# Kernel tuning notes

Measured on AMD Instinct MI355X. Metric: run time of the kernel, lower is better.

## Reference

```python
import jax, jax.numpy as jnp
import numpy as np

N_NODES = 100000
N_EDGES = 3200000
H, D = 3, 12  # heads, per-head dim; H*D == node_hidden_dim == 36
NEG_SLOPE = 0.2


def setup_inputs() -> dict:
    key = jax.random.key(0)
    ks = jax.random.split(key, 11)
    s = 0.1
    return {
        "node_features": jax.random.normal(ks[0], (N_NODES, 36), jnp.float32),
        "src": jax.random.randint(ks[1], (N_EDGES,), 0, N_NODES),
        "dst": jax.random.randint(ks[2], (N_EDGES,), 0, N_NODES),
        "lin0_w": jax.random.normal(ks[3], (36, 36), jnp.float32) * s,
        "lin0_b": jax.random.normal(ks[4], (36,), jnp.float32) * s,
        "fc_w": jax.random.normal(ks[5], (3, 36, 36), jnp.float32) * s,
        "attn_l": jax.random.normal(ks[6], (3, H, D), jnp.float32) * s,
        "attn_r": jax.random.normal(ks[7], (3, H, D), jnp.float32) * s,
        "gat_bias": jax.random.normal(ks[8], (3, 36), jnp.float32) * s,
        "out_w": jax.random.normal(ks[9], (36, 36), jnp.float32) * s,
        "out_b": jax.random.normal(ks[10], (36,), jnp.float32) * s,
    }


def _gat_layer(h, src, dst, fc_w, a_l, a_r, bias):
    n = h.shape[0]
    feat = (h @ fc_w).reshape(n, H, D)                      # (N,H,D)
    el = jnp.sum(feat * a_l, axis=-1)                       # (N,H)
    er = jnp.sum(feat * a_r, axis=-1)                       # (N,H)
    e = el[src] + er[dst]                                   # (E,H)
    e = jnp.where(e >= 0, e, NEG_SLOPE * e)                 # leaky_relu(0.2)
    # edge softmax over incoming edges of each dst node (numerically stable)
    m = jax.ops.segment_max(e, dst, num_segments=n)         # (N,H)
    m = jnp.where(jnp.isfinite(m), m, 0.0)                  # zero-degree guard
    ee = jnp.exp(e - m[dst])                                # (E,H)
    denom = jax.ops.segment_sum(ee, dst, num_segments=n)    # (N,H)
    alpha = ee / jnp.maximum(denom[dst], 1e-9)              # (E,H)
    msg = feat[src] * alpha[:, :, None]                     # (E,H,D)
    rst = jax.ops.segment_sum(msg, dst, num_segments=n)     # (N,H,D)
    # residual (Identity since in_feats == H*D) + bias, then ELU
    rst = rst + h.reshape(n, H, D) + bias.reshape(1, H, D)
    return jax.nn.elu(rst).reshape(n, H * D)


def reference(node_features, src, dst, lin0_w, lin0_b, fc_w, attn_l, attn_r, gat_bias, out_w, out_b):
    h = node_features @ lin0_w + lin0_b
    for l in range(3):
        h = _gat_layer(h, src, dst, fc_w[l], attn_l[l], attn_r[l], gat_bias[l])
    return h @ out_w + out_b
```

## Files before the change

### kernel.cpp

```cpp
#include <hip/hip_runtime.h>
#include <math.h>

#define HID 36
#define NH 3
#define HD 12
#define BSHIFT 13
#define NBUCK 13
#define PSHIFT 8
#define PCHUNK 8192
#define CSRCAP 4096

typedef _Float16 f16;
typedef unsigned short u16;


__global__ void hist2_kernel(const int* __restrict__ dst, int* __restrict__ M,
                             int E, int C, int np) {
    __shared__ int h[512];
    int t = threadIdx.x;
    int c = blockIdx.x;
    for (int i = t; i < 512; i += blockDim.x) h[i] = 0;
    __syncthreads();
    int i0 = c * PCHUNK;
    int i1 = min(i0 + PCHUNK, E);
    for (int i = i0 + t; i < i1; i += blockDim.x)
        atomicAdd(&h[dst[i] >> PSHIFT], 1);
    __syncthreads();
    for (int b = t; b < np; b += blockDim.x)
        M[(size_t)b * C + c] = h[b];
}

__global__ void base_scan_kernel(const int* __restrict__ M, int* __restrict__ BaseT,
                                 int* __restrict__ T, int C, int np) {
    __shared__ int tmp[512];
    int b = blockIdx.x;
    int t = threadIdx.x;
    int v = (t < C) ? M[(size_t)b * C + t] : 0;
    tmp[t] = v;
    __syncthreads();
    for (int ofs = 1; ofs < 512; ofs <<= 1) {
        int x = 0;
        if (t >= ofs) x = tmp[t - ofs];
        __syncthreads();
        tmp[t] += x;
        __syncthreads();
    }
    if (t < C) BaseT[(size_t)t * 512 + b] = tmp[t] - v;
    if (t == 511) T[b] = tmp[511];
}

__global__ void scan_small_kernel(const int* __restrict__ T, int* __restrict__ poff, int np) {
    __shared__ int tmp[512];
    int t = threadIdx.x;
    int v = (t < np) ? T[t] : 0;
    tmp[t] = v;
    __syncthreads();
    for (int ofs = 1; ofs < 512; ofs <<= 1) {
        int x = 0;
        if (t >= ofs) x = tmp[t - ofs];
        __syncthreads();
        tmp[t] += x;
        __syncthreads();
    }
    int excl = tmp[t] - v;
    if (t < np) poff[t] = excl;
    if (t == np - 1) poff[np] = excl + v;
}

__global__ void part_scatter_kernel(const int* __restrict__ src, const int* __restrict__ dst,
                                    const int* __restrict__ BaseT, const int* __restrict__ poff,
                                    int* __restrict__ part, int E, int np) {
    __shared__ int h[512];
    __shared__ int base[512];
    int t = threadIdx.x;
    int c = blockIdx.x;
    for (int i = t; i < 512; i += blockDim.x) h[i] = 0;
    for (int b = t; b < np; b += blockDim.x)
        base[b] = poff[b] + BaseT[(size_t)c * 512 + b];
    __syncthreads();
    int i0 = c * PCHUNK;
    int i1 = min(i0 + PCHUNK, E);
    for (int i = i0 + t; i < i1; i += blockDim.x) {
        int d = dst[i];
        int bin = d >> PSHIFT;
        int r = atomicAdd(&h[bin], 1);
        part[base[bin] + r] = (src[i] << PSHIFT) | (d & ((1 << PSHIFT) - 1));
    }
}

__global__ void bucket_csr_kernel(const int* __restrict__ part, const int* __restrict__ T,
                                  const int* __restrict__ poff,
                                  int* __restrict__ csr, int* __restrict__ off,
                                  u16* __restrict__ counts, int n, int E) {
    __shared__ int cnt[256 * NBUCK];
    __shared__ int psum[256];
    int p = blockIdx.x;
    int t = threadIdx.x;
    int dbase = p << PSHIFT;
    int nd = min(256, n - dbase);
    int nc = nd * NBUCK;
    for (int i = t; i < nc; i += blockDim.x) cnt[i] = 0;
    __syncthreads();
    int cnt_p = T[p];
    int e0 = poff[p];
    const int* pp = part + e0;
    for (int i = t; i < cnt_p; i += blockDim.x) {
        int e = pp[i];
        atomicAdd(&cnt[(e & 255) * NBUCK + ((e >> PSHIFT) >> BSHIFT)], 1);
    }
    __syncthreads();
    int sum = 0;
    if (t < nd) {
        for (int k = 0; k < NBUCK; ++k) {
            int c = cnt[t * NBUCK + k];
            cnt[t * NBUCK + k] = sum;
            sum += c;
        }
    }
    psum[t] = (t < nd) ? sum : 0;
    __syncthreads();
    for (int ofs = 1; ofs < 256; ofs <<= 1) {
        int x = 0;
        if (t >= ofs) x = psum[t - ofs];
        __syncthreads();
        psum[t] += x;
        __syncthreads();
    }
    int dexcl = (t > 0) ? psum[t - 1] : 0;
    int start = e0 + dexcl;
    if (t < nd) {
        for (int k = 0; k < NBUCK; ++k) cnt[t * NBUCK + k] += start;
        off[dbase + t] = start;
    }
    __syncthreads();
    for (int i = t; i < cnt_p; i += blockDim.x) {
        int e = pp[i];
        int s = e >> PSHIFT;
        int idx = (e & 255) * NBUCK + (s >> BSHIFT);
        int pos = atomicAdd(&cnt[idx], 1);
        csr[pos] = s * 48;
    }
    __syncthreads();
    if (t < nd) {
        union { u16 cc[16]; uint4 q[2]; } u;
        int prev = start;
        for (int k = 0; k < NBUCK; ++k) {
            int end = cnt[t * NBUCK + k];
            u.cc[k] = (u16)(end - prev);
            prev = end;
        }
        u.cc[13] = 0; u.cc[14] = 0; u.cc[15] = 0;
        uint4* cp = (uint4*)(counts + (size_t)(dbase + t) * 16);
        cp[0] = u.q[0];
        cp[1] = u.q[1];
    }
    if (p == 0 && t == 0) off[n] = E;
}


__device__ __forceinline__ void edge_accum(uint4 qa, uint4 qb, float ern,
                                           float& denom, float* acc) {
    union { uint4 q[2]; f16 hx[16]; } v;
    v.q[0] = qa;
    v.q[1] = qb;
    float e = (float)v.hx[12] + ern;
    e = (e >= 0.f) ? e : 0.2f * e;
    float w = __expf(e);
    denom += w;
#pragma unroll
    for (int k = 0; k < HD; ++k) acc[k] += w * (float)v.hx[k];
}

__global__ void lin0tr_kernel(const float* __restrict__ x, const float* __restrict__ w0,
                              const float* __restrict__ b0, const float* __restrict__ fcw,
                              const float* __restrict__ al, const float* __restrict__ ar,
                              float* __restrict__ h, f16* __restrict__ packed,
                              float* __restrict__ er, int n) {
    __shared__ float W0[HID * HID];
    __shared__ float W1[HID * HID];
    __shared__ float Bs[HID], ALs[HID], ARs[HID];
    int t = threadIdx.x;
    for (int i = t; i < HID * HID; i += 256) { W0[i] = w0[i]; W1[i] = fcw[i]; }
    if (t < HID) { Bs[t] = b0[t]; ALs[t] = al[t]; ARs[t] = ar[t]; }
    __syncthreads();
    int node = blockIdx.x * 256 + t;
    if (node >= n) return;
    const float4* xp = (const float4*)(x + (size_t)node * HID);
    float h0[HID];
#pragma unroll
    for (int j = 0; j < HID; ++j) h0[j] = Bs[j];
#pragma unroll
    for (int kk = 0; kk < HID / 4; ++kk) {
        float4 xv = xp[kk];
        const float* w = &W0[(4 * kk) * HID];
#pragma unroll
        for (int j = 0; j < HID; ++j)
            h0[j] += xv.x * w[j] + xv.y * w[HID + j] + xv.z * w[2 * HID + j] + xv.w * w[3 * HID + j];
    }
    float* hp = h + (size_t)node * HID;
#pragma unroll
    for (int j = 0; j < HID; ++j) hp[j] = h0[j];
    float feat[HID];
#pragma unroll
    for (int j = 0; j < HID; ++j) feat[j] = 0.f;
#pragma unroll
    for (int k = 0; k < HID; ++k) {
        float hv = h0[k];
        const float* w = &W1[k * HID];
#pragma unroll
        for (int j = 0; j < HID; ++j) feat[j] += hv * w[j];
    }
    union { f16 hx[48]; uint4 q[6]; } u;
#pragma unroll
    for (int hh = 0; hh < NH; ++hh) {
        float sl = 0.f, sr = 0.f;
#pragma unroll
        for (int d = 0; d < HD; ++d) {
            sl += feat[hh * HD + d] * ALs[hh * HD + d];
            sr += feat[hh * HD + d] * ARs[hh * HD + d];
        }
#pragma unroll
        for (int d = 0; d < HD; ++d) u.hx[hh * 16 + d] = (f16)feat[hh * HD + d];
        u.hx[hh * 16 + 12] = (f16)sl;
        u.hx[hh * 16 + 13] = (f16)0.f;
        u.hx[hh * 16 + 14] = (f16)0.f;
        u.hx[hh * 16 + 15] = (f16)0.f;
        er[node * NH + hh] = sr;
    }
    uint4* prow = (uint4*)(packed + (size_t)node * 48);
#pragma unroll
    for (int q = 0; q < 6; ++q) prow[q] = u.q[q];
}

__global__ void __launch_bounds__(192)
aggtr_kernel(const f16* __restrict__ packed_in, const float* __restrict__ er_in,
             const float* __restrict__ hcur, const u16* __restrict__ counts,
             const int* __restrict__ off, const int* __restrict__ csr,
             const float* __restrict__ bias, const float* __restrict__ wnext,
             const float* __restrict__ aln, const float* __restrict__ arn,
             float* __restrict__ hnext, f16* __restrict__ packed_out,
             float* __restrict__ er_out, int n) {
    __shared__ float Wsh[HID * HID];
    __shared__ float ALs[HID], ARs[HID];
    __shared__ int smbuf[CSRCAP];
    int t = threadIdx.x;
    for (int i = t; i < HID * HID; i += 192) Wsh[i] = wnext[i];
    if (t < HID) { ALs[t] = aln[t]; ARs[t] = arn[t]; }
    int ln = t / 3, hh = t - ln * 3;
    int nb0 = blockIdx.x * 64;
    int node = nb0 + ln;
    bool active = (node < n);

    int e0 = off[nb0];
    int e1 = off[min(nb0 + 64, n)];
    int span = e1 - e0;
    for (int i = t; i < span && i < CSRCAP; i += 192) smbuf[i] = csr[e0 + i];

    int j = 0;
    float ern = 0.f;
    union { u16 cc[16]; uint4 q[2]; } u;
    u.q[0] = make_uint4(0, 0, 0, 0);
    u.q[1] = make_uint4(0, 0, 0, 0);
    if (active) {
        j = off[node] - e0;
        ern = er_in[node * NH + hh];
        const uint4* cp = (const uint4*)(counts + (size_t)node * 16);
        u.q[0] = cp[0];
        u.q[1] = cp[1];
    }
    const f16* pb = packed_in + hh * 16;
    __syncthreads();

    float denom = 0.f;
    float acc[HD];
#pragma unroll
    for (int k = 0; k < HD; ++k) acc[k] = 0.f;

    for (int kb = 0; kb < NBUCK; ++kb) {
        int c = u.cc[kb];
        for (; c >= 2; c -= 2, j += 2) {
            int o0 = (j < CSRCAP) ? smbuf[j] : csr[e0 + j];
            int o1 = (j + 1 < CSRCAP) ? smbuf[j + 1] : csr[e0 + j + 1];
            const uint4* r0 = (const uint4*)(pb + o0);
            const uint4* r1 = (const uint4*)(pb + o1);
            uint4 a0 = r0[0], b0 = r0[1];
            uint4 a1 = r1[0], b1 = r1[1];
            edge_accum(a0, b0, ern, denom, acc);
            edge_accum(a1, b1, ern, denom, acc);
        }
        if (c) {
            int o = (j < CSRCAP) ? smbuf[j] : csr[e0 + j];
            ++j;
            const uint4* r = (const uint4*)(pb + o);
            edge_accum(r[0], r[1], ern, denom, acc);
        }
        __syncthreads();
    }

    float* hsh = (float*)smbuf;
    float v[HD];
#pragma unroll
    for (int k = 0; k < HD; ++k) v[k] = 0.f;
    if (active) {
        float inv = 1.f / fmaxf(denom, 1e-9f);
        int base = node * HID + hh * HD;
        const float4* hc = (const float4*)(hcur + base);
        float4 h0 = hc[0], h1 = hc[1], h2 = hc[2];
        float hres[HD] = {h0.x, h0.y, h0.z, h0.w, h1.x, h1.y, h1.z, h1.w, h2.x, h2.y, h2.z, h2.w};
#pragma unroll
        for (int k = 0; k < HD; ++k) {
            float x = acc[k] * inv + hres[k] + bias[hh * HD + k];
            v[k] = (x > 0.f) ? x : expm1f(x);
        }
        float4* hp = (float4*)(hnext + base);
        hp[0] = make_float4(v[0], v[1], v[2], v[3]);
        hp[1] = make_float4(v[4], v[5], v[6], v[7]);
        hp[2] = make_float4(v[8], v[9], v[10], v[11]);
    }
#pragma unroll
    for (int k = 0; k < HD; ++k) hsh[ln * 37 + hh * HD + k] = v[k];
    __syncthreads();

    float feat[HD];
#pragma unroll
    for (int d = 0; d < HD; ++d) feat[d] = 0.f;
    const float* hrow = &hsh[ln * 37];
#pragma unroll 4
    for (int k = 0; k < HID; ++k) {
        float hv = hrow[k];
        const float* w = &Wsh[k * HID + hh * HD];
#pragma unroll
        for (int d = 0; d < HD; ++d) feat[d] += hv * w[d];
    }
    if (!active) return;
    float sl = 0.f, sr = 0.f;
#pragma unroll
    for (int d = 0; d < HD; ++d) {
        sl += feat[d] * ALs[hh * HD + d];
        sr += feat[d] * ARs[hh * HD + d];
    }
    union { f16 hx[16]; uint4 q[2]; } o;
#pragma unroll
    for (int d = 0; d < HD; ++d) o.hx[d] = (f16)feat[d];
    o.hx[12] = (f16)sl;
    o.hx[13] = (f16)0.f; o.hx[14] = (f16)0.f; o.hx[15] = (f16)0.f;
    uint4* prow = (uint4*)(packed_out + (size_t)node * 48 + hh * 16);
    prow[0] = o.q[0];
    prow[1] = o.q[1];
    er_out[node * NH + hh] = sr;
}

__global__ void __launch_bounds__(192)
aggout_kernel(const f16* __restrict__ packed_in, const float* __restrict__ er_in,
              const float* __restrict__ hcur, const u16* __restrict__ counts,
              const int* __restrict__ off, const int* __restrict__ csr,
              const float* __restrict__ bias, const float* __restrict__ ow,
              const float* __restrict__ ob, float* __restrict__ out, int n) {
    __shared__ float Wsh[HID * HID];
    __shared__ float OBs[HID];
    __shared__ int smbuf[CSRCAP];
    int t = threadIdx.x;
    for (int i = t; i < HID * HID; i += 192) Wsh[i] = ow[i];
    if (t < HID) OBs[t] = ob[t];
    int ln = t / 3, hh = t - ln * 3;
    int nb0 = blockIdx.x * 64;
    int node = nb0 + ln;
    bool active = (node < n);

    int e0 = off[nb0];
    int e1 = off[min(nb0 + 64, n)];
    int span = e1 - e0;
    for (int i = t; i < span && i < CSRCAP; i += 192) smbuf[i] = csr[e0 + i];

    int j = 0;
    float ern = 0.f;
    union { u16 cc[16]; uint4 q[2]; } u;
    u.q[0] = make_uint4(0, 0, 0, 0);
    u.q[1] = make_uint4(0, 0, 0, 0);
    if (active) {
        j = off[node] - e0;
        ern = er_in[node * NH + hh];
        const uint4* cp = (const uint4*)(counts + (size_t)node * 16);
        u.q[0] = cp[0];
        u.q[1] = cp[1];
    }
    const f16* pb = packed_in + hh * 16;
    __syncthreads();

    float denom = 0.f;
    float acc[HD];
#pragma unroll
    for (int k = 0; k < HD; ++k) acc[k] = 0.f;

    for (int kb = 0; kb < NBUCK; ++kb) {
        int c = u.cc[kb];
        for (; c >= 2; c -= 2, j += 2) {
            int o0 = (j < CSRCAP) ? smbuf[j] : csr[e0 + j];
            int o1 = (j + 1 < CSRCAP) ? smbuf[j + 1] : csr[e0 + j + 1];
            const uint4* r0 = (const uint4*)(pb + o0);
            const uint4* r1 = (const uint4*)(pb + o1);
            uint4 a0 = r0[0], b0 = r0[1];
            uint4 a1 = r1[0], b1 = r1[1];
            edge_accum(a0, b0, ern, denom, acc);
            edge_accum(a1, b1, ern, denom, acc);
        }
        if (c) {
            int o = (j < CSRCAP) ? smbuf[j] : csr[e0 + j];
            ++j;
            const uint4* r = (const uint4*)(pb + o);
            edge_accum(r[0], r[1], ern, denom, acc);
        }
        __syncthreads();
    }

    float* hsh = (float*)smbuf;
    float v[HD];
#pragma unroll
    for (int k = 0; k < HD; ++k) v[k] = 0.f;
    if (active) {
        float inv = 1.f / fmaxf(denom, 1e-9f);
        int base = node * HID + hh * HD;
        const float4* hc = (const float4*)(hcur + base);
        float4 h0 = hc[0], h1 = hc[1], h2 = hc[2];
        float hres[HD] = {h0.x, h0.y, h0.z, h0.w, h1.x, h1.y, h1.z, h1.w, h2.x, h2.y, h2.z, h2.w};
#pragma unroll
        for (int k = 0; k < HD; ++k) {
            float x = acc[k] * inv + hres[k] + bias[hh * HD + k];
            v[k] = (x > 0.f) ? x : expm1f(x);
        }
    }
#pragma unroll
    for (int k = 0; k < HD; ++k) hsh[ln * 37 + hh * HD + k] = v[k];
    __syncthreads();

    float feat[HD];
#pragma unroll
    for (int d = 0; d < HD; ++d) feat[d] = OBs[hh * HD + d];
    const float* hrow = &hsh[ln * 37];
#pragma unroll 4
    for (int k = 0; k < HID; ++k) {
        float hv = hrow[k];
        const float* w = &Wsh[k * HID + hh * HD];
#pragma unroll
        for (int d = 0; d < HD; ++d) feat[d] += hv * w[d];
    }
    if (!active) return;
    float4* op = (float4*)(out + (size_t)node * HID + hh * HD);
    op[0] = make_float4(feat[0], feat[1], feat[2], feat[3]);
    op[1] = make_float4(feat[4], feat[5], feat[6], feat[7]);
    op[2] = make_float4(feat[8], feat[9], feat[10], feat[11]);
}


extern "C" void kernel_launch(void* const* d_in, const int* in_sizes, int n_in,
                              void* d_out, int out_size, void* d_ws, size_t ws_size,
                              hipStream_t stream) {
    const float* xnf = (const float*)d_in[0];
    const int* src = (const int*)d_in[1];
    const int* dst = (const int*)d_in[2];
    const float* l0w = (const float*)d_in[3];
    const float* l0b = (const float*)d_in[4];
    const float* fcw = (const float*)d_in[5];
    const float* al  = (const float*)d_in[6];
    const float* ar  = (const float*)d_in[7];
    const float* gb  = (const float*)d_in[8];
    const float* ow  = (const float*)d_in[9];
    const float* ob  = (const float*)d_in[10];
    float* out = (float*)d_out;
    const int N = in_sizes[0] / HID;
    const int E = in_sizes[1];
    const int NP = (N + (1 << PSHIFT) - 1) >> PSHIFT;
    const int C = (E + PCHUNK - 1) / PCHUNK;

    char* p = (char*)d_ws;
    auto alloc = [&](size_t bytes) {
        char* r = p;
        p += (bytes + 255) & ~(size_t)255;
        return r;
    };
    int* part    = (int*)alloc((size_t)E * 4);
    int* M       = (int*)alloc((size_t)NP * C * 4);
    int* BaseT   = (int*)alloc((size_t)C * 512 * 4);
    int* T       = (int*)alloc((size_t)NP * 4);
    int* poff    = (int*)alloc((size_t)(NP + 1) * 4);
    int* off     = (int*)alloc((size_t)(N + 1) * 4);
    int* csr     = (int*)alloc((size_t)E * 4);
    u16* counts  = (u16*)alloc((size_t)N * 16 * 2);
    float* ha    = (float*)alloc((size_t)N * HID * 4);
    float* hb    = (float*)alloc((size_t)N * HID * 4);
    f16* pkA     = (f16*)alloc((size_t)N * 48 * 2);
    f16* pkB     = (f16*)alloc((size_t)N * 48 * 2);
    float* erA   = (float*)alloc((size_t)N * NH * 4);
    float* erB   = (float*)alloc((size_t)N * NH * 4);

    hist2_kernel<<<C, 256, 0, stream>>>(dst, M, E, C, NP);
    base_scan_kernel<<<NP, 512, 0, stream>>>(M, BaseT, T, C, NP);
    scan_small_kernel<<<1, 512, 0, stream>>>(T, poff, NP);
    part_scatter_kernel<<<C, 256, 0, stream>>>(src, dst, BaseT, poff, part, E, NP);
    bucket_csr_kernel<<<NP, 256, 0, stream>>>(part, T, poff, csr, off, counts, N, E);

    int nblk = (N + 255) / 256;
    int fblk = (N + 63) / 64;

    lin0tr_kernel<<<nblk, 256, 0, stream>>>(xnf, l0w, l0b, fcw, al, ar, ha, pkA, erA, N);

    aggtr_kernel<<<fblk, 192, 0, stream>>>(pkA, erA, ha, counts, off, csr, gb,
                                           fcw + (size_t)1 * HID * HID, al + HID, ar + HID,
                                           hb, pkB, erB, N);
    aggtr_kernel<<<fblk, 192, 0, stream>>>(pkB, erB, hb, counts, off, csr, gb + HID,
                                           fcw + (size_t)2 * HID * HID, al + 2 * HID, ar + 2 * HID,
                                           ha, pkA, erA, N);
    aggout_kernel<<<fblk, 192, 0, stream>>>(pkA, erA, ha, counts, off, csr, gb + 2 * HID,
                                            ow, ob, out, N);
}
```

Before: 403.9 us.

## Split each node's edge aggregation across two thread halves and coarsen source buckets

The aggregation kernels now launch 384 threads per 64-node block. Two threads share each (node, head) pair, each handling half the edges of every source bucket, and the second half's partial sums and denominator are combined through shared memory before the epilogue. The source-bucket granularity also changes from 13 buckets of 8192 nodes to 7 buckets of 16384 nodes, which means fewer per-bucket barriers at the cost of coarser gather locality. Each block gains an extra barrier and a shared-memory partial buffer, and the half-threads sit idle during the transform phase.

```diff
diff --git a/kernel.cpp b/kernel.cpp
--- a/kernel.cpp
+++ b/kernel.cpp
@@ -4,8 +4,8 @@
 #define HID 36
 #define NH 3
 #define HD 12
-#define BSHIFT 13
-#define NBUCK 13
+#define BSHIFT 14
+#define NBUCK 7
 #define PSHIFT 8
 #define PCHUNK 8192
 #define CSRCAP 4096
@@ -143,13 +143,14 @@
     __syncthreads();
     if (t < nd) {
         union { u16 cc[16]; uint4 q[2]; } u;
+        u.q[0] = make_uint4(0, 0, 0, 0);
+        u.q[1] = make_uint4(0, 0, 0, 0);
         int prev = start;
         for (int k = 0; k < NBUCK; ++k) {
             int end = cnt[t * NBUCK + k];
             u.cc[k] = (u16)(end - prev);
             prev = end;
         }
-        u.cc[13] = 0; u.cc[14] = 0; u.cc[15] = 0;
         uint4* cp = (uint4*)(counts + (size_t)(dbase + t) * 16);
         cp[0] = u.q[0];
         cp[1] = u.q[1];
@@ -232,7 +233,7 @@
     for (int q = 0; q < 6; ++q) prow[q] = u.q[q];
 }
 
-__global__ void __launch_bounds__(192)
+__global__ void __launch_bounds__(384)
 aggtr_kernel(const f16* __restrict__ packed_in, const float* __restrict__ er_in,
              const float* __restrict__ hcur, const u16* __restrict__ counts,
              const int* __restrict__ off, const int* __restrict__ csr,
@@ -243,10 +244,13 @@
     __shared__ float Wsh[HID * HID];
     __shared__ float ALs[HID], ARs[HID];
     __shared__ int smbuf[CSRCAP];
-    int t = threadIdx.x;
-    for (int i = t; i < HID * HID; i += 192) Wsh[i] = wnext[i];
+    __shared__ float prt[192 * 13];
+    int t = threadIdx.x;
+    for (int i = t; i < HID * HID; i += 384) Wsh[i] = wnext[i];
     if (t < HID) { ALs[t] = aln[t]; ARs[t] = arn[t]; }
-    int ln = t / 3, hh = t - ln * 3;
+    int s = (t >= 192) ? 1 : 0;
+    int id = t - s * 192;
+    int ln = id / 3, hh = id - ln * 3;
     int nb0 = blockIdx.x * 64;
     int node = nb0 + ln;
     bool active = (node < n);
@@ -254,7 +258,7 @@
     int e0 = off[nb0];
     int e1 = off[min(nb0 + 64, n)];
     int span = e1 - e0;
-    for (int i = t; i < span && i < CSRCAP; i += 192) smbuf[i] = csr[e0 + i];
+    for (int i = t; i < span && i < CSRCAP; i += 384) smbuf[i] = csr[e0 + i];
 
     int j = 0;
     float ern = 0.f;
@@ -278,9 +282,12 @@
 
     for (int kb = 0; kb < NBUCK; ++kb) {
         int c = u.cc[kb];
-        for (; c >= 2; c -= 2, j += 2) {
-            int o0 = (j < CSRCAP) ? smbuf[j] : csr[e0 + j];
-            int o1 = (j + 1 < CSRCAP) ? smbuf[j + 1] : csr[e0 + j + 1];
+        int c0 = (c + 1) >> 1;
+        int cs = s ? (c - c0) : c0;
+        int js = j + (s ? c0 : 0);
+        for (; cs >= 2; cs -= 2, js += 2) {
+            int o0 = (js < CSRCAP) ? smbuf[js] : csr[e0 + js];
+            int o1 = (js + 1 < CSRCAP) ? smbuf[js + 1] : csr[e0 + js + 1];
             const uint4* r0 = (const uint4*)(pb + o0);
             const uint4* r1 = (const uint4*)(pb + o1);
             uint4 a0 = r0[0], b0 = r0[1];
@@ -288,39 +295,54 @@
             edge_accum(a0, b0, ern, denom, acc);
             edge_accum(a1, b1, ern, denom, acc);
         }
-        if (c) {
-            int o = (j < CSRCAP) ? smbuf[j] : csr[e0 + j];
-            ++j;
+        if (cs) {
+            int o = (js < CSRCAP) ? smbuf[js] : csr[e0 + js];
             const uint4* r = (const uint4*)(pb + o);
             edge_accum(r[0], r[1], ern, denom, acc);
         }
-        __syncthreads();
-    }
-
+        j += c;
+        __syncthreads();
+    }
+
+    if (s) {
+        float* pp = &prt[id * 13];
+#pragma unroll
+        for (int k = 0; k < HD; ++k) pp[k] = acc[k];
+        pp[12] = denom;
+    }
+    __syncthreads();
     float* hsh = (float*)smbuf;
     float v[HD];
 #pragma unroll
     for (int k = 0; k < HD; ++k) v[k] = 0.f;
-    if (active) {
-        float inv = 1.f / fmaxf(denom, 1e-9f);
-        int base = node * HID + hh * HD;
-        const float4* hc = (const float4*)(hcur + base);
-        float4 h0 = hc[0], h1 = hc[1], h2 = hc[2];
-        float hres[HD] = {h0.x, h0.y, h0.z, h0.w, h1.x, h1.y, h1.z, h1.w, h2.x, h2.y, h2.z, h2.w};
-#pragma unroll
-        for (int k = 0; k < HD; ++k) {
-            float x = acc[k] * inv + hres[k] + bias[hh * HD + k];
-            v[k] = (x > 0.f) ? x : expm1f(x);
-        }
-        float4* hp = (float4*)(hnext + base);
-        hp[0] = make_float4(v[0], v[1], v[2], v[3]);
-        hp[1] = make_float4(v[4], v[5], v[6], v[7]);
-        hp[2] = make_float4(v[8], v[9], v[10], v[11]);
-    }
-#pragma unroll
-    for (int k = 0; k < HD; ++k) hsh[ln * 37 + hh * HD + k] = v[k];
-    __syncthreads();
-
+    if (!s) {
+        const float* pp = &prt[id * 13];
+#pragma unroll
+        for (int k = 0; k < HD; ++k) acc[k] += pp[k];
+        denom += pp[12];
+        if (active) {
+            float inv = 1.f / fmaxf(denom, 1e-9f);
+            int base = node * HID + hh * HD;
+            const float4* hc = (const float4*)(hcur + base);
+            float4 h0 = hc[0], h1 = hc[1], h2 = hc[2];
+            float hres[HD] = {h0.x, h0.y, h0.z, h0.w, h1.x, h1.y, h1.z, h1.w,
+                              h2.x, h2.y, h2.z, h2.w};
+#pragma unroll
+            for (int k = 0; k < HD; ++k) {
+                float x = acc[k] * inv + hres[k] + bias[hh * HD + k];
+                v[k] = (x > 0.f) ? x : expm1f(x);
+            }
+            float4* hp = (float4*)(hnext + base);
+            hp[0] = make_float4(v[0], v[1], v[2], v[3]);
+            hp[1] = make_float4(v[4], v[5], v[6], v[7]);
+            hp[2] = make_float4(v[8], v[9], v[10], v[11]);
+        }
+#pragma unroll
+        for (int k = 0; k < HD; ++k) hsh[ln * 37 + hh * HD + k] = v[k];
+    }
+    __syncthreads();
+
+    if (s || !active) return;
     float feat[HD];
 #pragma unroll
     for (int d = 0; d < HD; ++d) feat[d] = 0.f;
@@ -332,7 +354,6 @@
 #pragma unroll
         for (int d = 0; d < HD; ++d) feat[d] += hv * w[d];
     }
-    if (!active) return;
     float sl = 0.f, sr = 0.f;
 #pragma unroll
     for (int d = 0; d < HD; ++d) {
@@ -350,7 +371,7 @@
     er_out[node * NH + hh] = sr;
 }
 
-__global__ void __launch_bounds__(192)
+__global__ void __launch_bounds__(384)
 aggout_kernel(const f16* __restrict__ packed_in, const float* __restrict__ er_in,
               const float* __restrict__ hcur, const u16* __restrict__ counts,
               const int* __restrict__ off, const int* __restrict__ csr,
@@ -359,10 +380,13 @@
     __shared__ float Wsh[HID * HID];
     __shared__ float OBs[HID];
     __shared__ int smbuf[CSRCAP];
-    int t = threadIdx.x;
-    for (int i = t; i < HID * HID; i += 192) Wsh[i] = ow[i];
+    __shared__ float prt[192 * 13];
+    int t = threadIdx.x;
+    for (int i = t; i < HID * HID; i += 384) Wsh[i] = ow[i];
     if (t < HID) OBs[t] = ob[t];
-    int ln = t / 3, hh = t - ln * 3;
+    int s = (t >= 192) ? 1 : 0;
+    int id = t - s * 192;
+    int ln = id / 3, hh = id - ln * 3;
     int nb0 = blockIdx.x * 64;
     int node = nb0 + ln;
     bool active = (node < n);
@@ -370,7 +394,7 @@
     int e0 = off[nb0];
     int e1 = off[min(nb0 + 64, n)];
     int span = e1 - e0;
-    for (int i = t; i < span && i < CSRCAP; i += 192) smbuf[i] = csr[e0 + i];
+    for (int i = t; i < span && i < CSRCAP; i += 384) smbuf[i] = csr[e0 + i];
 
     int j = 0;
     float ern = 0.f;
@@ -394,9 +418,12 @@
 
     for (int kb = 0; kb < NBUCK; ++kb) {
         int c = u.cc[kb];
-        for (; c >= 2; c -= 2, j += 2) {
-            int o0 = (j < CSRCAP) ? smbuf[j] : csr[e0 + j];
-            int o1 = (j + 1 < CSRCAP) ? smbuf[j + 1] : csr[e0 + j + 1];
+        int c0 = (c + 1) >> 1;
+        int cs = s ? (c - c0) : c0;
+        int js = j + (s ? c0 : 0);
+        for (; cs >= 2; cs -= 2, js += 2) {
+            int o0 = (js < CSRCAP) ? smbuf[js] : csr[e0 + js];
+            int o1 = (js + 1 < CSRCAP) ? smbuf[js + 1] : csr[e0 + js + 1];
             const uint4* r0 = (const uint4*)(pb + o0);
             const uint4* r1 = (const uint4*)(pb + o1);
             uint4 a0 = r0[0], b0 = r0[1];
@@ -404,35 +431,50 @@
             edge_accum(a0, b0, ern, denom, acc);
             edge_accum(a1, b1, ern, denom, acc);
         }
-        if (c) {
-            int o = (j < CSRCAP) ? smbuf[j] : csr[e0 + j];
-            ++j;
+        if (cs) {
+            int o = (js < CSRCAP) ? smbuf[js] : csr[e0 + js];
             const uint4* r = (const uint4*)(pb + o);
             edge_accum(r[0], r[1], ern, denom, acc);
         }
-        __syncthreads();
-    }
-
+        j += c;
+        __syncthreads();
+    }
+
+    if (s) {
+        float* pp = &prt[id * 13];
+#pragma unroll
+        for (int k = 0; k < HD; ++k) pp[k] = acc[k];
+        pp[12] = denom;
+    }
+    __syncthreads();
     float* hsh = (float*)smbuf;
     float v[HD];
 #pragma unroll
     for (int k = 0; k < HD; ++k) v[k] = 0.f;
-    if (active) {
-        float inv = 1.f / fmaxf(denom, 1e-9f);
-        int base = node * HID + hh * HD;
-        const float4* hc = (const float4*)(hcur + base);
-        float4 h0 = hc[0], h1 = hc[1], h2 = hc[2];
-        float hres[HD] = {h0.x, h0.y, h0.z, h0.w, h1.x, h1.y, h1.z, h1.w, h2.x, h2.y, h2.z, h2.w};
-#pragma unroll
-        for (int k = 0; k < HD; ++k) {
-            float x = acc[k] * inv + hres[k] + bias[hh * HD + k];
-            v[k] = (x > 0.f) ? x : expm1f(x);
-        }
-    }
-#pragma unroll
-    for (int k = 0; k < HD; ++k) hsh[ln * 37 + hh * HD + k] = v[k];
-    __syncthreads();
-
+    if (!s) {
+        const float* pp = &prt[id * 13];
+#pragma unroll
+        for (int k = 0; k < HD; ++k) acc[k] += pp[k];
+        denom += pp[12];
+        if (active) {
+            float inv = 1.f / fmaxf(denom, 1e-9f);
+            int base = node * HID + hh * HD;
+            const float4* hc = (const float4*)(hcur + base);
+            float4 h0 = hc[0], h1 = hc[1], h2 = hc[2];
+            float hres[HD] = {h0.x, h0.y, h0.z, h0.w, h1.x, h1.y, h1.z, h1.w,
+                              h2.x, h2.y, h2.z, h2.w};
+#pragma unroll
+            for (int k = 0; k < HD; ++k) {
+                float x = acc[k] * inv + hres[k] + bias[hh * HD + k];
+                v[k] = (x > 0.f) ? x : expm1f(x);
+            }
+        }
+#pragma unroll
+        for (int k = 0; k < HD; ++k) hsh[ln * 37 + hh * HD + k] = v[k];
+    }
+    __syncthreads();
+
+    if (s || !active) return;
     float feat[HD];
 #pragma unroll
     for (int d = 0; d < HD; ++d) feat[d] = OBs[hh * HD + d];
@@ -444,7 +486,6 @@
 #pragma unroll
         for (int d = 0; d < HD; ++d) feat[d] += hv * w[d];
     }
-    if (!active) return;
     float4* op = (float4*)(out + (size_t)node * HID + hh * HD);
     op[0] = make_float4(feat[0], feat[1], feat[2], feat[3]);
     op[1] = make_float4(feat[4], feat[5], feat[6], feat[7]);
@@ -504,12 +545,12 @@
 
     lin0tr_kernel<<<nblk, 256, 0, stream>>>(xnf, l0w, l0b, fcw, al, ar, ha, pkA, erA, N);
 
-    aggtr_kernel<<<fblk, 192, 0, stream>>>(pkA, erA, ha, counts, off, csr, gb,
+    aggtr_kernel<<<fblk, 384, 0, stream>>>(pkA, erA, ha, counts, off, csr, gb,
                                            fcw + (size_t)1 * HID * HID, al + HID, ar + HID,
                                            hb, pkB, erB, N);
-    aggtr_kernel<<<fblk, 192, 0, stream>>>(pkB, erB, hb, counts, off, csr, gb + HID,
+    aggtr_kernel<<<fblk, 384, 0, stream>>>(pkB, erB, hb, counts, off, csr, gb + HID,
                                            fcw + (size_t)2 * HID * HID, al + 2 * HID, ar + 2 * HID,
                                            ha, pkA, erA, N);
-    aggout_kernel<<<fblk, 192, 0, stream>>>(pkA, erA, ha, counts, off, csr, gb + 2 * HID,
+    aggout_kernel<<<fblk, 384, 0, stream>>>(pkA, erA, ha, counts, off, csr, gb + 2 * HID,
                                             ow, ob, out, N);
 }
```

After: 409.7 us. Within noise of the previous version (+1.4%).
